# Performance work log

Hardware: AMD Instinct MI355X
Metric: run time of the kernel (lower is better)

Reference implementation:

```python
import jax, jax.numpy as jnp
import numpy as np

B = 512
MIRROR_C1_OFFSET = -1.2432432432432432

def make_ff(batch):
    ff = jnp.zeros((1, 1, 60, 60), jnp.float32)
    ff = ff.at[0, 0, :, 41:51].set(0.5)
    ff = ff.at[0, 0, :, 51:].set(1.0)
    return jnp.broadcast_to(ff, (batch, 1, 60, 60))

def conv_valid(x, w, b):
    y = jax.lax.conv_general_dilated(x, w, (1, 1), 'VALID',
                                     dimension_numbers=('NCHW', 'OIHW', 'NCHW'))
    return y + b[None, :, None, None]

def build_padded(x, h, ff):
    # (B,3,92,92) canvas with custom mirror padding (channel-dependent sign on left)
    b = x.shape[0]
    inner = jnp.concatenate([x, h, ff], axis=1)  # (B,3,60,60)
    h2 = jnp.zeros((b, 3, 92, 92), x.dtype)
    h2 = h2.at[:, :, 16:76, 16:76].set(inner)
    h2 = h2.at[:, :, 16:76, 76:].set(h2[:, :, 16:76, 60:76][..., ::-1])
    h2 = h2.at[:, :, 76:, 16:].set(h2[:, :, 60:76, 16:][:, :, ::-1, :])
    h2 = h2.at[:, :, :16, 16:].set(0.0)
    left = h2[:, :, :, 16:32][..., ::-1]  # mirror across col 16
    h2 = h2.at[:, 0, :, :16].set(left[:, 0])
    h2 = h2.at[:, 2, :, :16].set(left[:, 2])
    h2 = h2.at[:, 1, :, :16].set(MIRROR_C1_OFFSET - left[:, 1])
    return h2

def powerlayer(x, h, ff, w1, b1, w2, b2, w3, b3, w4, b4):
    h2 = build_padded(x, h, ff)
    h2 = jax.nn.relu(conv_valid(h2, w1, b1))  # (B,8,84,84)
    h2 = jax.nn.relu(conv_valid(h2, w2, b2))  # (B,8,76,76)
    h2 = jax.nn.relu(conv_valid(h2, w3, b3))  # (B,8,68,68)
    h2 = conv_valid(h2, w4, b4)               # (B,1,60,60)
    return h2

def setup_inputs() -> dict:
    key = jax.random.key(0)
    ks = jax.random.split(key, 10)
    x = jax.random.normal(ks[0], (B, 1, 60, 60), jnp.float32)
    fc_w = jax.random.normal(ks[1], (3600, 3600), jnp.float32) * (1.0 / 60.0)
    fc_b = jax.random.normal(ks[2], (3600,), jnp.float32) * 0.01
    w1 = jax.random.normal(ks[3], (8, 3, 9, 9), jnp.float32) * (1.0 / np.sqrt(3 * 81))
    bC1 = jnp.zeros((8,), jnp.float32)
    w2 = jax.random.normal(ks[4], (8, 8, 9, 9), jnp.float32) * (1.0 / np.sqrt(8 * 81))
    bC2 = jnp.zeros((8,), jnp.float32)
    w3 = jax.random.normal(ks[5], (8, 8, 9, 9), jnp.float32) * (1.0 / np.sqrt(8 * 81))
    bC3 = jnp.zeros((8,), jnp.float32)
    w4 = jax.random.normal(ks[6], (1, 8, 9, 9), jnp.float32) * (1.0 / np.sqrt(8 * 81))
    bC4 = jnp.zeros((1,), jnp.float32)
    return {"x": x, "fc_w": fc_w, "fc_b": fc_b,
            "w1": w1, "bC1": bC1, "w2": w2, "bC2": bC2,
            "w3": w3, "bC3": bC3, "w4": w4, "bC4": bC4}

def reference(x, fc_w, fc_b, w1, bC1, w2, bC2, w3, bC3, w4, bC4):
    b = x.shape[0]
    ff = make_ff(b)
    h = jax.nn.relu(x.reshape(b, 3600) @ fc_w.T + fc_b)
    h = h.reshape(b, 1, 60, 60)
    for _ in range(5):
        h = powerlayer(x, h, ff, w1, bC1, w2, bC2, w3, bC3, w4, bC4)
    return h.reshape(b, 60, 60)
```

## Files before the change

### kernel.cpp

```cpp
#include <hip/hip_runtime.h>

#define B_IMG 512
#define C1OFF (-1.2432432432432432f)

typedef __attribute__((ext_vector_type(2))) float f2;
typedef __attribute__((ext_vector_type(2), aligned(4))) float f2u;
typedef __attribute__((ext_vector_type(4))) float f4;
typedef __attribute__((ext_vector_type(4), aligned(4))) float f4u;

__device__ __forceinline__ float relu_(float v) { return v > 0.f ? v : 0.f; }
__device__ __forceinline__ f2 mk2(float a, float b) { f2 r; r[0] = a; r[1] = b; return r; }

__device__ __forceinline__ int swz_block(int bid, int nwg) {
    int q = nwg >> 3, r = nwg & 7;
    int xcd = bid & 7, idx = bid >> 3;
    return (xcd < r ? xcd * (q + 1) : r * (q + 1) + (xcd - r) * q) + idx;
}

__device__ __forceinline__ f2 pk_fma_sb0(f2 acc, f2 a, f2 b) {
    asm("v_pk_fma_f32 %0, %1, %2, %0 op_sel:[0,0,0] op_sel_hi:[0,1,1]"
        : "+v"(acc) : "s"(a), "v"(b));
    return acc;
}
__device__ __forceinline__ f2 pk_fma_sb1(f2 acc, f2 a, f2 b) {
    asm("v_pk_fma_f32 %0, %1, %2, %0 op_sel:[1,0,0] op_sel_hi:[1,1,1]"
        : "+v"(acc) : "s"(a), "v"(b));
    return acc;
}
__device__ __forceinline__ f2 pk_fma_vb0(f2 acc, f2 a, f2 b) {
    asm("v_pk_fma_f32 %0, %1, %2, %0 op_sel:[0,0,0] op_sel_hi:[0,1,1]"
        : "+v"(acc) : "v"(a), "v"(b));
    return acc;
}
__device__ __forceinline__ f2 pk_fma_vb1(f2 acc, f2 a, f2 b) {
    asm("v_pk_fma_f32 %0, %1, %2, %0 op_sel:[1,0,0] op_sel_hi:[1,1,1]"
        : "+v"(acc) : "v"(a), "v"(b));
    return acc;
}

__global__ __launch_bounds__(256) void fc_kernel(
    const float* __restrict__ X, const float* __restrict__ W,
    const float* __restrict__ Bv, float* __restrict__ H)
{
    __shared__ __align__(16) float As[16][68];
    __shared__ __align__(16) float Bs[16][68];
    const int tid = threadIdx.x;
    const int m0 = blockIdx.y * 64;
    const int n0 = blockIdx.x * 64;
    const int tm = tid >> 4, tn = tid & 15;
    const int lr = tid >> 2;
    const int lk = (tid & 3) << 2;
    const bool bvalid = (n0 + lr) < 3600;
    const float* Arow = X + (size_t)(m0 + lr) * 3600 + lk;
    const float* Brow = W + (size_t)(bvalid ? (n0 + lr) : 0) * 3600 + lk;
    f2 acc2[4][2] = {};
    for (int k0 = 0; k0 < 3600; k0 += 16) {
        float4 av = *(const float4*)(Arow + k0);
        float4 bv = make_float4(0.f, 0.f, 0.f, 0.f);
        if (bvalid) bv = *(const float4*)(Brow + k0);
        __syncthreads();
        As[lk + 0][lr] = av.x; As[lk + 1][lr] = av.y;
        As[lk + 2][lr] = av.z; As[lk + 3][lr] = av.w;
        Bs[lk + 0][lr] = bv.x; Bs[lk + 1][lr] = bv.y;
        Bs[lk + 2][lr] = bv.z; Bs[lk + 3][lr] = bv.w;
        __syncthreads();
        #pragma unroll
        for (int kk = 0; kk < 16; ++kk) {
            f2 a01 = *(const f2*)&As[kk][tm << 2];
            f2 a23 = *(const f2*)&As[kk][(tm << 2) + 2];
            f2 b01 = *(const f2*)&Bs[kk][tn << 2];
            f2 b23 = *(const f2*)&Bs[kk][(tn << 2) + 2];
            acc2[0][0] = pk_fma_vb0(acc2[0][0], a01, b01);
            acc2[0][1] = pk_fma_vb0(acc2[0][1], a01, b23);
            acc2[1][0] = pk_fma_vb1(acc2[1][0], a01, b01);
            acc2[1][1] = pk_fma_vb1(acc2[1][1], a01, b23);
            acc2[2][0] = pk_fma_vb0(acc2[2][0], a23, b01);
            acc2[2][1] = pk_fma_vb0(acc2[2][1], a23, b23);
            acc2[3][0] = pk_fma_vb1(acc2[3][0], a23, b01);
            acc2[3][1] = pk_fma_vb1(acc2[3][1], a23, b23);
        }
    }
    #pragma unroll
    for (int i = 0; i < 4; ++i) {
        int m = m0 + (tm << 2) + i;
        float vals[4] = { acc2[i][0][0], acc2[i][0][1],
                          acc2[i][1][0], acc2[i][1][1] };
        #pragma unroll
        for (int j = 0; j < 4; ++j) {
            int n = n0 + (tn << 2) + j;
            if (n < 3600)
                H[(size_t)m * 3600 + n] = relu_(vals[j] + Bv[n]);
        }
    }
}

__global__ __launch_bounds__(256) void prep_pk(
    const float* __restrict__ w, int OC, int IC, f2* __restrict__ out)
{
    int n = IC * 9 * OC * 5;
    for (int t = threadIdx.x + blockIdx.x * 256; t < n; t += gridDim.x * 256) {
        int m = t % 5; int rest = t / 5;
        int oc = rest % OC; rest /= OC;
        int ky = rest % 9; int ic = rest / 9;
        const float* ws = w + (((size_t)oc * IC + ic) * 9 + ky) * 9;
        float lo = ws[2 * m];
        float hi = (2 * m + 1 < 9) ? ws[2 * m + 1] : 0.f;
        out[t] = mk2(lo, hi);
    }
}

__device__ __forceinline__ float pad_core(const float* __restrict__ xb,
                                          const float* __restrict__ hb,
                                          int ch, int r, int c)
{
    if (r < 16) return 0.f;
    int rr = (r <= 75) ? r : (151 - r);
    int cc = (c <= 75) ? c : (151 - c);
    int i = rr - 16, j = cc - 16;
    if (ch == 0) return xb[i * 60 + j];
    if (ch == 1) return hb[i * 60 + j];
    return (j >= 51) ? 1.0f : ((j >= 41) ? 0.5f : 0.0f);
}

__device__ __forceinline__ float pad_val(const float* __restrict__ xb,
                                         const float* __restrict__ hb,
                                         int ch, int r, int c)
{
    if (c >= 16) return pad_core(xb, hb, ch, r, c);
    float v = pad_core(xb, hb, ch, r, 31 - c);
    return (ch == 1) ? (C1OFF - v) : v;
}

__global__ __launch_bounds__(256) void pad_kernel(
    const float* __restrict__ x, const float* __restrict__ h,
    float* __restrict__ pad)
{
    const int b = blockIdx.x;
    const float* xb = x + (size_t)b * 3600;
    const float* hb = h + (size_t)b * 3600;
    float* pb = pad + (size_t)b * (3 * 92 * 92);
    for (int i = threadIdx.x; i < 3 * 92 * 92; i += 256) {
        int ch = i / 8464;
        int rem = i - ch * 8464;
        int r = rem / 92;
        int c = rem - r * 92;
        pb[i] = pad_val(xb, hb, ch, r, c);
    }
}

#define LOADROW(RE, SH, KY)                                                   \
    do {                                                                      \
        const float* row_ = rp + (KY) * IW;                                   \
        f4 e0_ = *(const f4*)(row_);                                          \
        f4 e1_ = *(const f4*)(row_ + 4);                                      \
        f4 e2_ = *(const f4*)(row_ + 8);                                      \
        f4u s0_ = *(const f4u*)(row_ + 1);                                    \
        f4u s1_ = *(const f4u*)(row_ + 5);                                    \
        f2u s2_ = *(const f2u*)(row_ + 9);                                    \
        RE[0] = mk2(e0_[0], e0_[1]); RE[1] = mk2(e0_[2], e0_[3]);             \
        RE[2] = mk2(e1_[0], e1_[1]); RE[3] = mk2(e1_[2], e1_[3]);             \
        RE[4] = mk2(e2_[0], e2_[1]); RE[5] = mk2(e2_[2], e2_[3]);             \
        SH[0] = mk2(s0_[0], s0_[1]); SH[1] = mk2(s0_[2], s0_[3]);             \
        SH[2] = mk2(s1_[0], s1_[1]); SH[3] = mk2(s1_[2], s1_[3]);             \
        SH[4] = mk2(s2_[0], s2_[1]);                                          \
    } while (0)

#define FMASTEP(TRE, TSH, BRE, BSH, KY)                                       \
    do {                                                                      \
        const f2* wq_ = wq0 + (KY) * OC * 5;                                  \
        _Pragma("unroll")                                                     \
        for (int oc = 0; oc < OC; ++oc) {                                     \
            const f2* w5_ = wq_ + oc * 5;                                     \
            _Pragma("unroll")                                                 \
            for (int m = 0; m < 4; ++m) {                                     \
                f2 w_ = w5_[m];                                               \
                acc[oc][0][0] = pk_fma_sb0(acc[oc][0][0], w_, TRE[m]);        \
                acc[oc][0][0] = pk_fma_sb1(acc[oc][0][0], w_, TSH[m]);        \
                acc[oc][0][1] = pk_fma_sb0(acc[oc][0][1], w_, TRE[m + 1]);    \
                acc[oc][0][1] = pk_fma_sb1(acc[oc][0][1], w_, TSH[m + 1]);    \
                acc[oc][1][0] = pk_fma_sb0(acc[oc][1][0], w_, BRE[m]);        \
                acc[oc][1][0] = pk_fma_sb1(acc[oc][1][0], w_, BSH[m]);        \
                acc[oc][1][1] = pk_fma_sb0(acc[oc][1][1], w_, BRE[m + 1]);    \
                acc[oc][1][1] = pk_fma_sb1(acc[oc][1][1], w_, BSH[m + 1]);    \
            }                                                                 \
            f2 w4_ = w5_[4];                                                  \
            acc[oc][0][0] = pk_fma_sb0(acc[oc][0][0], w4_, TRE[4]);           \
            acc[oc][0][1] = pk_fma_sb0(acc[oc][0][1], w4_, TRE[5]);           \
            acc[oc][1][0] = pk_fma_sb0(acc[oc][1][0], w4_, BRE[4]);           \
            acc[oc][1][1] = pk_fma_sb0(acc[oc][1][1], w4_, BRE[5]);           \
        }                                                                     \
    } while (0)

#define STEP(TRE, TSH, BRE, BSH, KY)                                          \
    do { LOADROW(BRE, BSH, (KY) + 1); FMASTEP(TRE, TSH, BRE, BSH, KY); } while (0)

template<int IC, int OC, int IH, bool RELU>
__global__ __launch_bounds__(256, 2) void convP2(
    const float* __restrict__ in, const f2* __restrict__ wpk,
    const float* __restrict__ bias, float* __restrict__ out, int total)
{
    constexpr int IW = IH, OH = IH - 8, OW = OH;
    constexpr int NGX = OW / 4, NGY = OH / 2, NPB = NGX * NGY;
    const int sb = swz_block(blockIdx.x, gridDim.x);
    const int p0 = sb * 256 + threadIdx.x;
    const bool act = (p0 < total);
    const int p = act ? p0 : (total - 1);
    const int b = p / NPB;
    const int rem = p - b * NPB;
    const int gy = rem / NGX;
    const int gx = rem - gy * NGX;
    const int oy = gy * 2, x0 = gx * 4;
    const float* ib = in + (size_t)b * IC * IH * IW + (size_t)oy * IW + x0;

    f2 acc[OC][2][2];
    #pragma unroll
    for (int oc = 0; oc < OC; ++oc) {
        float bv = bias[oc];
        acc[oc][0][0] = mk2(bv, bv); acc[oc][0][1] = mk2(bv, bv);
        acc[oc][1][0] = mk2(bv, bv); acc[oc][1][1] = mk2(bv, bv);
    }

    #pragma unroll 1
    for (int ic = 0; ic < IC; ++ic) {
        const float* rp = ib + (size_t)ic * IH * IW;
        const f2* wq0 = wpk + (size_t)ic * 9 * OC * 5;
        f2 reA[6], shA[5], reB[6], shB[5];
        LOADROW(reA, shA, 0);
        STEP(reA, shA, reB, shB, 0);
        STEP(reB, shB, reA, shA, 1);
        STEP(reA, shA, reB, shB, 2);
        STEP(reB, shB, reA, shA, 3);
        STEP(reA, shA, reB, shB, 4);
        STEP(reB, shB, reA, shA, 5);
        STEP(reA, shA, reB, shB, 6);
        STEP(reB, shB, reA, shA, 7);
        STEP(reA, shA, reB, shB, 8);
    }

    if (act) {
        #pragma unroll
        for (int oc = 0; oc < OC; ++oc) {
            float* ob = out + ((size_t)b * OC + oc) * (OH * OW)
                        + (size_t)oy * OW + x0;
            float v0 = acc[oc][0][0][0], v1 = acc[oc][0][0][1];
            float v2 = acc[oc][0][1][0], v3 = acc[oc][0][1][1];
            float u0 = acc[oc][1][0][0], u1 = acc[oc][1][0][1];
            float u2 = acc[oc][1][1][0], u3 = acc[oc][1][1][1];
            if (RELU) {
                v0 = relu_(v0); v1 = relu_(v1); v2 = relu_(v2); v3 = relu_(v3);
                u0 = relu_(u0); u1 = relu_(u1); u2 = relu_(u2); u3 = relu_(u3);
            }
            *(float4*)&ob[0]  = make_float4(v0, v1, v2, v3);
            *(float4*)&ob[OW] = make_float4(u0, u1, u2, u3);
        }
    }
}

extern "C" void kernel_launch(void* const* d_in, const int* in_sizes, int n_in,
                              void* d_out, int out_size, void* d_ws, size_t ws_size,
                              hipStream_t stream)
{
    const float* x   = (const float*)d_in[0];
    const float* fcw = (const float*)d_in[1];
    const float* fcb = (const float*)d_in[2];
    const float* w1  = (const float*)d_in[3];
    const float* b1  = (const float*)d_in[4];
    const float* w2  = (const float*)d_in[5];
    const float* b2  = (const float*)d_in[6];
    const float* w3  = (const float*)d_in[7];
    const float* b3  = (const float*)d_in[8];
    const float* w4  = (const float*)d_in[9];
    const float* b4  = (const float*)d_in[10];

    float* h = (float*)d_out;

    f2* wp1 = (f2*)d_ws;
    f2* wp2 = wp1 + 4096;
    f2* wp3 = wp2 + 4096;
    f2* wp4 = wp3 + 4096;
    float* fbase = (float*)((char*)d_ws + 131072);
    size_t avail = (ws_size - 131072) / sizeof(float);

    const size_t PADN = 3 * 92 * 92;
    const size_t T1N  = 8 * 84 * 84;
    const size_t T2N  = 8 * 76 * 76;
    size_t per_img = PADN + T1N + T2N;
    int CH = (int)(avail / per_img);
    if (CH > B_IMG) CH = B_IMG;
    if (CH < 1) CH = 1;
    float* pad = fbase;
    float* t1  = pad + (size_t)CH * PADN;
    float* t2  = t1 + (size_t)CH * T1N;

    prep_pk<<<5, 256, 0, stream>>>(w1, 8, 3, wp1);
    prep_pk<<<12, 256, 0, stream>>>(w2, 8, 8, wp2);
    prep_pk<<<12, 256, 0, stream>>>(w3, 8, 8, wp3);
    prep_pk<<<2, 256, 0, stream>>>(w4, 1, 8, wp4);

    fc_kernel<<<dim3(57, 8), 256, 0, stream>>>(x, fcw, fcb, h);

    for (int it = 0; it < 5; ++it) {
        for (int c0 = 0; c0 < B_IMG; c0 += CH) {
            int cn = (B_IMG - c0) < CH ? (B_IMG - c0) : CH;
            pad_kernel<<<cn, 256, 0, stream>>>(x + (size_t)c0 * 3600,
                                               h + (size_t)c0 * 3600, pad);
            int t1n = cn * 882, t2n = cn * 722, t3n = cn * 578, t4n = cn * 450;
            convP2<3, 8, 92, true><<<(t1n + 255) / 256, 256, 0, stream>>>(
                pad, wp1, b1, t1, t1n);
            convP2<8, 8, 84, true><<<(t2n + 255) / 256, 256, 0, stream>>>(
                t1, wp2, b2, t2, t2n);
            convP2<8, 8, 76, true><<<(t3n + 255) / 256, 256, 0, stream>>>(
                t2, wp3, b3, t1, t3n);
            convP2<8, 1, 68, false><<<(t4n + 255) / 256, 256, 0, stream>>>(
                t1, wp4, b4, h + (size_t)c0 * 3600, t4n);
        }
    }
}
```

Before: 3.900 ms.

## Hoist loop-invariant x/ff conv1 contribution, add 1-row conv variant for middle layers

```diff
diff --git a/kernel.cpp b/kernel.cpp
--- a/kernel.cpp
+++ b/kernel.cpp
@@ -131,20 +131,124 @@
     return (ch == 1) ? (C1OFF - v) : v;
 }
 
-__global__ __launch_bounds__(256) void pad_kernel(
-    const float* __restrict__ x, const float* __restrict__ h,
-    float* __restrict__ pad)
+#define PADN 25392
+#define CH1OFF 8464
+
+__global__ __launch_bounds__(256) void pad02_kernel(
+    const float* __restrict__ x, float* __restrict__ pad)
 {
     const int b = blockIdx.x;
     const float* xb = x + (size_t)b * 3600;
-    const float* hb = h + (size_t)b * 3600;
-    float* pb = pad + (size_t)b * (3 * 92 * 92);
-    for (int i = threadIdx.x; i < 3 * 92 * 92; i += 256) {
-        int ch = i / 8464;
-        int rem = i - ch * 8464;
+    float* pb = pad + (size_t)b * PADN;
+    for (int i = threadIdx.x; i < 2 * 8464; i += 256) {
+        int cs = i / 8464;
+        int rem = i - cs * 8464;
         int r = rem / 92;
         int c = rem - r * 92;
-        pb[i] = pad_val(xb, hb, ch, r, c);
+        int ch = cs * 2;
+        pb[(size_t)ch * CH1OFF + rem] = pad_val(xb, nullptr, ch, r, c);
+    }
+}
+
+__global__ __launch_bounds__(256) void padh_kernel(
+    const float* __restrict__ h, float* __restrict__ pad)
+{
+    const int b = blockIdx.x;
+    const float* hb = h + (size_t)b * 3600;
+    float* pb = pad + (size_t)b * PADN + CH1OFF;
+    for (int i = threadIdx.x; i < 8464; i += 256) {
+        int r = i / 92;
+        int c = i - r * 92;
+        pb[i] = pad_val(nullptr, hb, 1, r, c);
+    }
+}
+
+template<int IC, int OC, int IH, bool RELU, bool INIT>
+__global__ __launch_bounds__(256, 3) void convP(
+    const float* __restrict__ in, const f2* __restrict__ wpk,
+    const float* __restrict__ bias, const float* __restrict__ basep,
+    float* __restrict__ out, int total, int istride, int chstride, int wstride)
+{
+    constexpr int IW = IH, OH = IH - 8, OW = OH;
+    constexpr int NGX = OW / 4, NPB = OH * NGX;
+    const int sb = swz_block(blockIdx.x, gridDim.x);
+    const int p0 = sb * 256 + threadIdx.x;
+    const bool act = (p0 < total);
+    const int p = act ? p0 : (total - 1);
+    const int b = p / NPB;
+    const int rem = p - b * NPB;
+    const int oy = rem / NGX;
+    const int x0 = (rem - oy * NGX) * 4;
+    const float* ib = in + (size_t)b * istride + (size_t)oy * IW + x0;
+
+    f2 acc[OC][2];
+    if (INIT) {
+        #pragma unroll
+        for (int oc = 0; oc < OC; ++oc) {
+            const float* bp = basep + ((size_t)b * OC + oc) * (OH * OW)
+                              + (size_t)oy * OW + x0;
+            f4 v = *(const f4*)bp;
+            acc[oc][0] = mk2(v[0], v[1]);
+            acc[oc][1] = mk2(v[2], v[3]);
+        }
+    } else {
+        #pragma unroll
+        for (int oc = 0; oc < OC; ++oc) {
+            float bv = bias[oc];
+            acc[oc][0] = mk2(bv, bv);
+            acc[oc][1] = mk2(bv, bv);
+        }
+    }
+
+    #pragma unroll 1
+    for (int ic = 0; ic < IC; ++ic) {
+        const float* rp = ib + (size_t)ic * chstride;
+        const f2* wq0 = wpk + (size_t)ic * wstride;
+        #pragma unroll
+        for (int ky = 0; ky < 9; ++ky) {
+            const float* row = rp + ky * IW;
+            f4 e0 = *(const f4*)(row);
+            f4 e1 = *(const f4*)(row + 4);
+            f4 e2 = *(const f4*)(row + 8);
+            f4u s0 = *(const f4u*)(row + 1);
+            f4u s1 = *(const f4u*)(row + 5);
+            f2u s2 = *(const f2u*)(row + 9);
+            f2 re[6], sh[5];
+            re[0] = mk2(e0[0], e0[1]); re[1] = mk2(e0[2], e0[3]);
+            re[2] = mk2(e1[0], e1[1]); re[3] = mk2(e1[2], e1[3]);
+            re[4] = mk2(e2[0], e2[1]); re[5] = mk2(e2[2], e2[3]);
+            sh[0] = mk2(s0[0], s0[1]); sh[1] = mk2(s0[2], s0[3]);
+            sh[2] = mk2(s1[0], s1[1]); sh[3] = mk2(s1[2], s1[3]);
+            sh[4] = mk2(s2[0], s2[1]);
+            const f2* wq = wq0 + ky * OC * 5;
+            #pragma unroll
+            for (int oc = 0; oc < OC; ++oc) {
+                const f2* w5 = wq + oc * 5;
+                #pragma unroll
+                for (int m = 0; m < 4; ++m) {
+                    f2 w = w5[m];
+                    acc[oc][0] = pk_fma_sb0(acc[oc][0], w, re[m]);
+                    acc[oc][0] = pk_fma_sb1(acc[oc][0], w, sh[m]);
+                    acc[oc][1] = pk_fma_sb0(acc[oc][1], w, re[m + 1]);
+                    acc[oc][1] = pk_fma_sb1(acc[oc][1], w, sh[m + 1]);
+                }
+                f2 w4v = w5[4];
+                acc[oc][0] = pk_fma_sb0(acc[oc][0], w4v, re[4]);
+                acc[oc][1] = pk_fma_sb0(acc[oc][1], w4v, re[5]);
+            }
+        }
+    }
+
+    if (act) {
+        #pragma unroll
+        for (int oc = 0; oc < OC; ++oc) {
+            float* ob = out + ((size_t)b * OC + oc) * (OH * OW)
+                        + (size_t)oy * OW + x0;
+            float v0 = acc[oc][0][0], v1 = acc[oc][0][1];
+            float v2 = acc[oc][1][0], v3 = acc[oc][1][1];
+            if (RELU) { v0 = relu_(v0); v1 = relu_(v1); v2 = relu_(v2); v3 = relu_(v3); }
+            *(float4*)ob = make_float4(v0, v1, v2, v3);
+        }
     }
 }
 
@@ -194,10 +298,11 @@
 #define STEP(TRE, TSH, BRE, BSH, KY)                                          \
     do { LOADROW(BRE, BSH, (KY) + 1); FMASTEP(TRE, TSH, BRE, BSH, KY); } while (0)
 
-template<int IC, int OC, int IH, bool RELU>
+template<int IC, int OC, int IH, bool RELU, bool INIT>
 __global__ __launch_bounds__(256, 2) void convP2(
     const float* __restrict__ in, const f2* __restrict__ wpk,
-    const float* __restrict__ bias, float* __restrict__ out, int total)
+    const float* __restrict__ bias, const float* __restrict__ basep,
+    float* __restrict__ out, int total, int istride, int chstride, int wstride)
 {
     constexpr int IW = IH, OH = IH - 8, OW = OH;
     constexpr int NGX = OW / 4, NGY = OH / 2, NPB = NGX * NGY;
@@ -210,20 +315,32 @@
     const int gy = rem / NGX;
     const int gx = rem - gy * NGX;
     const int oy = gy * 2, x0 = gx * 4;
-    const float* ib = in + (size_t)b * IC * IH * IW + (size_t)oy * IW + x0;
+    const float* ib = in + (size_t)b * istride + (size_t)oy * IW + x0;
 
     f2 acc[OC][2][2];
-    #pragma unroll
-    for (int oc = 0; oc < OC; ++oc) {
-        float bv = bias[oc];
-        acc[oc][0][0] = mk2(bv, bv); acc[oc][0][1] = mk2(bv, bv);
-        acc[oc][1][0] = mk2(bv, bv); acc[oc][1][1] = mk2(bv, bv);
+    if (INIT) {
+        #pragma unroll
+        for (int oc = 0; oc < OC; ++oc) {
+            const float* bp = basep + ((size_t)b * OC + oc) * (OH * OW)
+                              + (size_t)oy * OW + x0;
+            f4 v0 = *(const f4*)bp;
+            f4 v1 = *(const f4*)(bp + OW);
+            acc[oc][0][0] = mk2(v0[0], v0[1]); acc[oc][0][1] = mk2(v0[2], v0[3]);
+            acc[oc][1][0] = mk2(v1[0], v1[1]); acc[oc][1][1] = mk2(v1[2], v1[3]);
+        }
+    } else {
+        #pragma unroll
+        for (int oc = 0; oc < OC; ++oc) {
+            float bv = bias[oc];
+            acc[oc][0][0] = mk2(bv, bv); acc[oc][0][1] = mk2(bv, bv);
+            acc[oc][1][0] = mk2(bv, bv); acc[oc][1][1] = mk2(bv, bv);
+        }
     }
 
     #pragma unroll 1
     for (int ic = 0; ic < IC; ++ic) {
-        const float* rp = ib + (size_t)ic * IH * IW;
-        const f2* wq0 = wpk + (size_t)ic * 9 * OC * 5;
+        const float* rp = ib + (size_t)ic * chstride;
+        const f2* wq0 = wpk + (size_t)ic * wstride;
         f2 reA[6], shA[5], reB[6], shB[5];
         LOADROW(reA, shA, 0);
         STEP(reA, shA, reB, shB, 0);
@@ -281,16 +398,16 @@
     float* fbase = (float*)((char*)d_ws + 131072);
     size_t avail = (ws_size - 131072) / sizeof(float);
 
-    const size_t PADN = 3 * 92 * 92;
-    const size_t T1N  = 8 * 84 * 84;
-    const size_t T2N  = 8 * 76 * 76;
-    size_t per_img = PADN + T1N + T2N;
-    int CH = (int)(avail / per_img);
-    if (CH > B_IMG) CH = B_IMG;
-    if (CH < 1) CH = 1;
-    float* pad = fbase;
-    float* t1  = pad + (size_t)CH * PADN;
-    float* t2  = t1 + (size_t)CH * T1N;
+    const size_t T1N = 8 * 84 * 84;
+    const size_t T2N = 8 * 76 * 76;
+    size_t per_img = PADN + T1N + T1N + T2N;
+    int CHN = (int)(avail / per_img);
+    if (CHN > B_IMG) CHN = B_IMG;
+    if (CHN < 1) CHN = 1;
+    float* pad  = fbase;
+    float* bse  = pad + (size_t)CHN * PADN;
+    float* t1   = bse + (size_t)CHN * T1N;
+    float* t2   = t1 + (size_t)CHN * T1N;
 
     prep_pk<<<5, 256, 0, stream>>>(w1, 8, 3, wp1);
     prep_pk<<<12, 256, 0, stream>>>(w2, 8, 8, wp2);
@@ -299,20 +416,27 @@
 
     fc_kernel<<<dim3(57, 8), 256, 0, stream>>>(x, fcw, fcb, h);
 
-    for (int it = 0; it < 5; ++it) {
-        for (int c0 = 0; c0 < B_IMG; c0 += CH) {
-            int cn = (B_IMG - c0) < CH ? (B_IMG - c0) : CH;
-            pad_kernel<<<cn, 256, 0, stream>>>(x + (size_t)c0 * 3600,
-                                               h + (size_t)c0 * 3600, pad);
-            int t1n = cn * 882, t2n = cn * 722, t3n = cn * 578, t4n = cn * 450;
-            convP2<3, 8, 92, true><<<(t1n + 255) / 256, 256, 0, stream>>>(
-                pad, wp1, b1, t1, t1n);
-            convP2<8, 8, 84, true><<<(t2n + 255) / 256, 256, 0, stream>>>(
-                t1, wp2, b2, t2, t2n);
-            convP2<8, 8, 76, true><<<(t3n + 255) / 256, 256, 0, stream>>>(
-                t2, wp3, b3, t1, t3n);
-            convP2<8, 1, 68, false><<<(t4n + 255) / 256, 256, 0, stream>>>(
-                t1, wp4, b4, h + (size_t)c0 * 3600, t4n);
-        }
-    }
-}
+    for (int c0 = 0; c0 < B_IMG; c0 += CHN) {
+        int cn = (B_IMG - c0) < CHN ? (B_IMG - c0) : CHN;
+        pad02_kernel<<<cn, 256, 0, stream>>>(x + (size_t)c0 * 3600, pad);
+        int tb = cn * 882;
+        convP2<2, 8, 92, false, false><<<(tb + 255) / 256, 256, 0, stream>>>(
+            pad, wp1, b1, nullptr, bse, tb, PADN, 2 * CH1OFF, 2 * 360);
+        for (int it = 0; it < 5; ++it) {
+            padh_kernel<<<cn, 256, 0, stream>>>(h + (size_t)c0 * 3600, pad);
+            int t1n = cn * 882;
+            int t2n = cn * 1444;
+            int t3n = cn * 1156;
+            int t4n = cn * 450;
+            convP2<1, 8, 92, true, true><<<(t1n + 255) / 256, 256, 0, stream>>>(
+                pad + CH1OFF, wp1 + 360, nullptr, bse, t1, t1n, PADN, 0, 0);
+            convP<8, 8, 84, true, false><<<(t2n + 255) / 256, 256, 0, stream>>>(
+                t1, wp2, b2, nullptr, t2, t2n, (int)T1N, 84 * 84, 360);
+            convP<8, 8, 76, true, false><<<(t3n + 255) / 256, 256, 0, stream>>>(
+                t2, wp3, b3, nullptr, t1, t3n, (int)T2N, 76 * 76, 360);
+            convP2<8, 1, 68, false, false><<<(t4n + 255) / 256, 256, 0, stream>>>(
+                t1, wp4, b4, nullptr, h + (size_t)c0 * 3600, t4n,
+                8 * 68 * 68, 68 * 68, 45);
+        }
+    }
+}
```

Result: no change. 3.917 ms (+0.4%).
